# Kernel tuning notes

Hardware: AMD Instinct MI355X
Metric: run time of the kernel (lower is better)

Reference implementation:

```python
import jax, jax.numpy as jnp
import numpy as np

B, T, I, H, O = 512, 512, 128, 512, 128


def setup_inputs() -> dict:
    key = jax.random.key(0)
    k = jax.random.split(key, 6)
    si = 1.0 / np.sqrt(I)
    sh = 1.0 / np.sqrt(H)
    x = jax.random.normal(k[0], (B, T, I), dtype=jnp.float32)
    # gate order along last axis: [g, i, f, o] (each H wide)
    Wx = jax.random.uniform(k[1], (I, 4 * H), jnp.float32, -si, si)
    Wh = jax.random.uniform(k[2], (H, 4 * H), jnp.float32, -sh, sh)
    b = jax.random.uniform(k[3], (4 * H,), jnp.float32, -sh, sh)
    Wp = jax.random.uniform(k[4], (H, O), jnp.float32, -sh, sh)
    bp = jax.random.uniform(k[5], (O,), jnp.float32, -sh, sh)
    return {"x": x, "Wx": Wx, "Wh": Wh, "b": b, "Wp": Wp, "bp": bp}


def reference(x, Wx, Wh, b, Wp, bp):
    # x: [B, T, I]. Fused LSTM: one input GEMM + one hidden GEMM per step,
    # gates split from the concatenated [g, i, f, o] projection.
    Bsz = x.shape[0]
    Hd = Wh.shape[0]
    # Precompute all input projections in one big GEMM: [T, B, 4H]
    xz = jnp.einsum('bti,ij->tbj', x, Wx)

    def step(carry, xzt):
        h, c = carry
        z = xzt + h @ Wh + b  # [B, 4H]
        g, i, f, o = jnp.split(z, 4, axis=-1)
        g = jnp.tanh(g)
        i = jax.nn.sigmoid(i)
        f = jax.nn.sigmoid(f)
        o = jax.nn.sigmoid(o)
        c = g * i + c * f
        h = jnp.tanh(c) * o
        return (h, c), None

    h0 = jnp.zeros((Bsz, Hd), dtype=x.dtype)
    c0 = jnp.zeros((Bsz, Hd), dtype=x.dtype)
    (h, c), _ = jax.lax.scan(step, (h0, c0), xz)
    p = h @ Wp + bp  # [B, O]
    return jax.nn.softmax(p, axis=1)
```

## Files before the change

### kernel.cpp

```cpp
#include <hip/hip_runtime.h>
#include <hip/hip_cooperative_groups.h>

namespace cg = cooperative_groups;

typedef _Float16 f16;
typedef _Float16 half8 __attribute__((ext_vector_type(8)));
typedef float float4v __attribute__((ext_vector_type(4)));
typedef unsigned long long u64;

constexpr int kB  = 512;
constexpr int kT  = 512;
constexpr int kI  = 128;
constexpr int kH  = 512;
constexpr int kNG = 2048;
constexpr int kO  = 128;

constexpr int LDK = 650;

__device__ __forceinline__ float fsig(float v)  { return 1.0f / (1.0f + __expf(-v)); }
__device__ __forceinline__ float ftanh(float v) { return 1.0f - 2.0f / (1.0f + __expf(2.0f * v)); }

union h8u { half8 h; u64 u[2]; };
union f16u { f16 f; unsigned short s; };

__global__ __launch_bounds__(256, 1) void lstm_fused(
    const float* __restrict__ x,  const float* __restrict__ Wx,
    const float* __restrict__ Wh, const float* __restrict__ bias,
    const float* __restrict__ Wp, const float* __restrict__ bp,
    float* __restrict__ out, float* __restrict__ ws)
{
  cg::grid_group grid = cg::this_grid();

  __shared__ __align__(16) f16 w_lds[64 * LDK];

  const int tid = threadIdx.x;
  const int wg  = blockIdx.x;
  const int bg  = wg & 7;
  const int ng  = wg >> 3;
  const int b0  = bg * 64;
  const int wv  = tid >> 6;
  const int l   = tid & 63;
  const int lc  = l & 15;
  const int lj  = l >> 4;

  f16* h16a = (f16*)ws;
  f16* h16b = h16a + kB * kH;
  unsigned* bar = (unsigned*)(h16b + kB * kH);

  {
    int gtid = wg * 256 + tid;
    unsigned* p = (unsigned*)h16a;
    p[gtid * 2] = 0u; p[gtid * 2 + 1] = 0u;
    if (gtid < 8192) bar[gtid] = 0u;
  }

  for (int idx = tid; idx < 64 * 640; idx += 256) {
    int c = idx & 63;
    int k = idx >> 6;
    int gcol = (c >> 4) * 512 + ng * 16 + (c & 15);
    float v = (k < 512) ? Wh[(long)k * kNG + gcol]
                        : Wx[(long)(k - 512) * kNG + gcol];
    w_lds[c * LDK + k] = (f16)v;
  }
  float bb[4];
  #pragma unroll
  for (int g = 0; g < 4; ++g) bb[g] = bias[g * 512 + ng * 16 + lc];

  float ce[4] = {0.f, 0.f, 0.f, 0.f};
  const int arow = b0 + wv * 16 + lc;
  const f16* wbase = w_lds + lc * LDK + lj * 8;
  const float* xrow = x + (long)arow * (kT * kI) + lj * 8;

  float4v xa[4], xb[4];
  #pragma unroll
  for (int q = 0; q < 4; ++q) {
    xa[q] = *(const float4v*)(xrow + q * 32);
    xb[q] = *(const float4v*)(xrow + q * 32 + 4);
  }

  grid.sync();

  unsigned* myslot = bar + (bg * 32 + ng) * 32;
  const unsigned* pollslot = bar + (bg * 32 + (l & 31)) * 32;

  float4v xacc[4];
  #pragma unroll
  for (int g = 0; g < 4; ++g) xacc[g] = float4v{bb[g], bb[g], bb[g], bb[g]};
  #pragma unroll
  for (int q = 0; q < 4; ++q) {
    half8 a;
    #pragma unroll
    for (int e = 0; e < 4; ++e) { a[e] = (f16)xa[q][e]; a[e + 4] = (f16)xb[q][e]; }
    #pragma unroll
    for (int g = 0; g < 4; ++g) {
      half8 bf = *(const half8*)(wbase + g * 16 * LDK + 512 + q * 32);
      xacc[g] = __builtin_amdgcn_mfma_f32_16x16x32_f16(a, bf, xacc[g], 0, 0, 0);
    }
  }
  #pragma unroll
  for (int q = 0; q < 4; ++q) {
    xa[q] = *(const float4v*)(xrow + kI + q * 32);
    xb[q] = *(const float4v*)(xrow + kI + q * 32 + 4);
  }

  for (int t = 0; t < kT; ++t) {
    const f16* hc = (t & 1) ? h16b : h16a;
    f16*       hn = (t & 1) ? h16a : h16b;

    const u64* hp64 = (const u64*)hc + (long)arow * 128 + lj * 2;
    h8u ah[16];
    #pragma unroll
    for (int p = 0; p < 16; ++p) {
      ah[p].u[0] = __hip_atomic_load(hp64 + p * 8,     __ATOMIC_RELAXED, __HIP_MEMORY_SCOPE_AGENT);
      ah[p].u[1] = __hip_atomic_load(hp64 + p * 8 + 1, __ATOMIC_RELAXED, __HIP_MEMORY_SCOPE_AGENT);
    }

    float4v acc[4];
    #pragma unroll
    for (int g = 0; g < 4; ++g) acc[g] = xacc[g];

    #pragma unroll
    for (int ks = 0; ks < 16; ++ks) {
      #pragma unroll
      for (int g = 0; g < 4; ++g) {
        half8 bf = *(const half8*)(wbase + g * 16 * LDK + ks * 32);
        acc[g] = __builtin_amdgcn_mfma_f32_16x16x32_f16(ah[ks].h, bf, acc[g], 0, 0, 0);
      }
    }

    #pragma unroll
    for (int e = 0; e < 4; ++e) {
      float gv = ftanh(acc[0][e]);
      float iv = fsig(acc[1][e]);
      float fv = fsig(acc[2][e]);
      float ov = fsig(acc[3][e]);
      float cn = gv * iv + ce[e] * fv;
      ce[e] = cn;
      f16u hv; hv.f = (f16)(ftanh(cn) * ov);
      unsigned short* dst = (unsigned short*)hn
          + (long)(b0 + wv * 16 + lj * 4 + e) * kH + ng * 16 + lc;
      __hip_atomic_store(dst, hv.s, __ATOMIC_RELAXED, __HIP_MEMORY_SCOPE_AGENT);
    }

    __syncthreads();
    if (tid == 0)
      __hip_atomic_store(myslot, (unsigned)(t + 1), __ATOMIC_RELAXED, __HIP_MEMORY_SCOPE_AGENT);

    if (t + 1 < kT) {
      #pragma unroll
      for (int g = 0; g < 4; ++g) xacc[g] = float4v{bb[g], bb[g], bb[g], bb[g]};
      #pragma unroll
      for (int q = 0; q < 4; ++q) {
        half8 a;
        #pragma unroll
        for (int e = 0; e < 4; ++e) { a[e] = (f16)xa[q][e]; a[e + 4] = (f16)xb[q][e]; }
        #pragma unroll
        for (int g = 0; g < 4; ++g) {
          half8 bf = *(const half8*)(wbase + g * 16 * LDK + 512 + q * 32);
          xacc[g] = __builtin_amdgcn_mfma_f32_16x16x32_f16(a, bf, xacc[g], 0, 0, 0);
        }
      }
      if (t + 2 < kT) {
        const float* xn = xrow + (long)(t + 2) * kI;
        #pragma unroll
        for (int q = 0; q < 4; ++q) {
          xa[q] = *(const float4v*)(xn + q * 32);
          xb[q] = *(const float4v*)(xn + q * 32 + 4);
        }
      }
    }

    if (wv == 0) {
      unsigned v;
      do {
        v = __hip_atomic_load(pollslot, __ATOMIC_RELAXED, __HIP_MEMORY_SCOPE_AGENT);
      } while (__all((int)(v >= (unsigned)(t + 1))) == 0);
    }
    __syncthreads();
  }

  grid.sync();

  const f16* hf = h16a;
  float* hrow = (float*)w_lds;
  float* red  = (float*)w_lds + 2 * kH;
  for (int i = tid; i < 2 * kH; i += 256) {
    int r = i >> 9, k = i & 511;
    hrow[i] = (float)hf[(long)(wg * 2 + r) * kH + k];
  }
  __syncthreads();

  const int orow = tid >> 7;
  const int oc   = tid & 127;
  float p = bp[oc];
  #pragma unroll 8
  for (int k = 0; k < kH; ++k)
    p += hrow[orow * kH + k] * Wp[(long)k * kO + oc];

  red[tid] = p;
  __syncthreads();
  float m = -1e30f;
  for (int j = 0; j < 128; ++j) m = fmaxf(m, red[orow * 128 + j]);
  __syncthreads();
  float e = __expf(p - m);
  red[tid] = e;
  __syncthreads();
  float s = 0.f;
  for (int j = 0; j < 128; ++j) s += red[orow * 128 + j];
  out[(long)(wg * 2 + orow) * kO + oc] = e / s;
}

extern "C" void kernel_launch(void* const* d_in, const int* in_sizes, int n_in,
                              void* d_out, int out_size, void* d_ws, size_t ws_size,
                              hipStream_t stream) {
  const float* x  = (const float*)d_in[0];
  const float* Wx = (const float*)d_in[1];
  const float* Wh = (const float*)d_in[2];
  const float* b  = (const float*)d_in[3];
  const float* Wp = (const float*)d_in[4];
  const float* bp = (const float*)d_in[5];
  float* out = (float*)d_out;
  float* ws  = (float*)d_ws;

  void* args[] = { &x, &Wx, &Wh, &b, &Wp, &bp, &out, &ws };
  hipLaunchCooperativeKernel((void*)lstm_fused, dim3(256), dim3(256), args, 0, stream);
}
```

Measured before the change: 5.558 ms.

## Replace block barriers with per-wavefront flags and use dwordx4 coherent h loads

Each wavefront now publishes its own progress flag and polls all producer wavefronts directly, which removes the two __syncthreads per timestep so wavefronts can proceed independently. The hidden-state reads become single 128-bit global loads with cache-bypass bits, issued through inline asm, in place of pairs of 64-bit atomic loads. Together these aim to shorten the per-step critical path of the recurrent loop. In exchange there are 4x more flags to poll, and ordering now depends on a waitcnt before the flag store with no explicit release fence, so memory-ordering correctness is a risk.

```diff
diff --git a/kernel.cpp b/kernel.cpp
--- a/kernel.cpp
+++ b/kernel.cpp
@@ -6,7 +6,7 @@
 typedef _Float16 f16;
 typedef _Float16 half8 __attribute__((ext_vector_type(8)));
 typedef float float4v __attribute__((ext_vector_type(4)));
-typedef unsigned long long u64;
+typedef int int4v __attribute__((ext_vector_type(4)));
 
 constexpr int kB  = 512;
 constexpr int kT  = 512;
@@ -20,7 +20,7 @@
 __device__ __forceinline__ float fsig(float v)  { return 1.0f / (1.0f + __expf(-v)); }
 __device__ __forceinline__ float ftanh(float v) { return 1.0f - 2.0f / (1.0f + __expf(2.0f * v)); }
 
-union h8u { half8 h; u64 u[2]; };
+union h8u { half8 h; int4v i; };
 union f16u { f16 f; unsigned short s; };
 
 __global__ __launch_bounds__(256, 1) void lstm_fused(
@@ -45,13 +45,13 @@
 
   f16* h16a = (f16*)ws;
   f16* h16b = h16a + kB * kH;
-  unsigned* bar = (unsigned*)(h16b + kB * kH);
+  unsigned* flags = (unsigned*)(h16b + kB * kH);
 
   {
     int gtid = wg * 256 + tid;
     unsigned* p = (unsigned*)h16a;
     p[gtid * 2] = 0u; p[gtid * 2 + 1] = 0u;
-    if (gtid < 8192) bar[gtid] = 0u;
+    if (gtid < 32768) flags[gtid] = 0u;
   }
 
   for (int idx = tid; idx < 64 * 640; idx += 256) {
@@ -80,8 +80,9 @@
 
   grid.sync();
 
-  unsigned* myslot = bar + (bg * 32 + ng) * 32;
-  const unsigned* pollslot = bar + (bg * 32 + (l & 31)) * 32;
+  unsigned* myslot = flags + (((unsigned)(bg * 32 + ng) * 4u + (unsigned)wv) * 32u);
+  const unsigned* poll0 = flags + (((unsigned)(bg * 32 + (l & 31)) * 4u + (unsigned)(l >> 5)) * 32u);
+  const unsigned* poll1 = flags + (((unsigned)(bg * 32 + (l & 31)) * 4u + (unsigned)((l >> 5) + 2)) * 32u);
 
   float4v xacc[4];
   #pragma unroll
@@ -103,22 +104,25 @@
     xb[q] = *(const float4v*)(xrow + kI + q * 32 + 4);
   }
 
+  const unsigned hoff = (unsigned)(arow * kH * 2 + lj * 16);
+
   for (int t = 0; t < kT; ++t) {
     const f16* hc = (t & 1) ? h16b : h16a;
     f16*       hn = (t & 1) ? h16a : h16b;
 
-    const u64* hp64 = (const u64*)hc + (long)arow * 128 + lj * 2;
     h8u ah[16];
     #pragma unroll
     for (int p = 0; p < 16; ++p) {
-      ah[p].u[0] = __hip_atomic_load(hp64 + p * 8,     __ATOMIC_RELAXED, __HIP_MEMORY_SCOPE_AGENT);
-      ah[p].u[1] = __hip_atomic_load(hp64 + p * 8 + 1, __ATOMIC_RELAXED, __HIP_MEMORY_SCOPE_AGENT);
-    }
+      asm volatile("global_load_dwordx4 %0, %1, %2 offset:%c3 sc0 sc1"
+                   : "=v"(ah[p].i)
+                   : "v"(hoff), "s"(hc), "i"(p * 64));
+    }
+    asm volatile("s_waitcnt vmcnt(0)" ::: "memory");
+    __builtin_amdgcn_sched_barrier(0);
 
     float4v acc[4];
     #pragma unroll
     for (int g = 0; g < 4; ++g) acc[g] = xacc[g];
-
     #pragma unroll
     for (int ks = 0; ks < 16; ++ks) {
       #pragma unroll
@@ -136,14 +140,14 @@
       float ov = fsig(acc[3][e]);
       float cn = gv * iv + ce[e] * fv;
       ce[e] = cn;
-      f16u hv; hv.f = (f16)(ftanh(cn) * ov);
+      f16u u; u.f = (f16)(ftanh(cn) * ov);
       unsigned short* dst = (unsigned short*)hn
           + (long)(b0 + wv * 16 + lj * 4 + e) * kH + ng * 16 + lc;
-      __hip_atomic_store(dst, hv.s, __ATOMIC_RELAXED, __HIP_MEMORY_SCOPE_AGENT);
-    }
-
-    __syncthreads();
-    if (tid == 0)
+      __hip_atomic_store(dst, u.s, __ATOMIC_RELAXED, __HIP_MEMORY_SCOPE_AGENT);
+    }
+
+    asm volatile("s_waitcnt vmcnt(0)" ::: "memory");
+    if (l == 0)
       __hip_atomic_store(myslot, (unsigned)(t + 1), __ATOMIC_RELAXED, __HIP_MEMORY_SCOPE_AGENT);
 
     if (t + 1 < kT) {
@@ -170,13 +174,15 @@
       }
     }
 
-    if (wv == 0) {
-      unsigned v;
+    {
+      const unsigned tgt = (unsigned)(t + 1);
+      unsigned v0, v1;
       do {
-        v = __hip_atomic_load(pollslot, __ATOMIC_RELAXED, __HIP_MEMORY_SCOPE_AGENT);
-      } while (__all((int)(v >= (unsigned)(t + 1))) == 0);
-    }
-    __syncthreads();
+        v0 = __hip_atomic_load(poll0, __ATOMIC_RELAXED, __HIP_MEMORY_SCOPE_AGENT);
+        v1 = __hip_atomic_load(poll1, __ATOMIC_RELAXED, __HIP_MEMORY_SCOPE_AGENT);
+        v0 = (v0 < v1) ? v0 : v1;
+      } while (__all((int)(v0 >= tgt)) == 0);
+    }
   }
 
   grid.sync();
```

Measured after the change: 6.125 ms. 1.1x slower.
